# Kernel optimization log

Measured on AMD Instinct MI355X. Metric: run time of the kernel, lower is better.

## Reference

```python
import jax, jax.numpy as jnp
import numpy as np

B = 4096
D = 1024
NUM_CLASSES = 100
TEMPERATURE = 0.5
EPS = 1e-12  # matches F.normalize default eps


def setup_inputs() -> dict:
    key = jax.random.key(0)
    k1, k2, k3 = jax.random.split(key, 3)
    emb_i = jax.random.normal(k1, (B, D), dtype=jnp.float32)
    emb_j = jax.random.normal(k2, (B, D), dtype=jnp.float32)
    labels = jax.random.randint(k3, (B,), 0, NUM_CLASSES, dtype=jnp.int32)
    return {"emb_i": emb_i, "emb_j": emb_j, "labels": labels}


def _l2_normalize(x):
    # F.normalize(x, dim=1): x / max(||x||, eps)
    n = jnp.sqrt(jnp.sum(x * x, axis=1, keepdims=True))
    return x / jnp.maximum(n, EPS)


def reference(emb_i, emb_j, labels):
    z_i = _l2_normalize(emb_i)
    z_j = _l2_normalize(emb_j)
    reps = jnp.concatenate([z_i, z_j], axis=0)          # [2B, D]
    # cosine similarity of already-unit vectors == dot product (GEMM instead
    # of the O(N^2 D) broadcasted elementwise form in the torch code)
    sim = jnp.einsum("nd,md->nm", reps, reps)           # [2B, 2B]

    n2 = 2 * B
    neg_mask = 1.0 - jnp.eye(n2, dtype=sim.dtype)       # exclude self-pairs
    label_t = jnp.concatenate([labels, labels], axis=0)  # [2B]
    ws = (label_t[:, None] == label_t[None, :]).astype(sim.dtype) * neg_mask

    e = jnp.exp(sim / TEMPERATURE)                      # [2B, 2B]
    nominator = jnp.sum(ws * e, axis=1)                 # [2B]
    denominator = jnp.sum(neg_mask * e, axis=1)         # [2B]
    loss_partial = -jnp.log(nominator / denominator)
    return jnp.sum(loss_partial) / (2 * B)
```

## Files before the change

kernel.cpp:

```cpp
#include <hip/hip_runtime.h>
#include <hip/hip_bf16.h>
#include <hip/hip_fp8.h>


#define BHALF 4096
#define N2 8192
#define DK 1024
#define DKB 512
#define TILE 128
#define BKB 64
#define NTILE 64
#define NBLK 2080

typedef __attribute__((ext_vector_type(16))) float f32x16;
typedef __attribute__((ext_vector_type(4))) int v4i;
typedef __attribute__((ext_vector_type(8))) int v8i;
typedef unsigned char u8;
typedef unsigned short u16;

#define EXP_SCALE4 0.0028177637517362566f
#define UNIT_SCALE 0x7f7f7f7f

#define WAITVM(n) asm volatile("s_waitcnt vmcnt(" #n ")" ::: "memory")
#define BAR()     asm volatile("s_barrier" ::: "memory")

static __device__ __forceinline__ unsigned nib4(float x) {
    unsigned s = (__builtin_bit_cast(unsigned, x) >> 31) << 3;
    float a = fminf(fabsf(x), 6.0f);
    unsigned c;
    if (a < 2.0f)      c = (unsigned)lrintf(a * 2.0f);
    else if (a < 4.0f) c = (unsigned)lrintf(a) + 2u;
    else               c = (a < 5.0f) ? 6u : 7u;
    return s | c;
}

__global__ __launch_bounds__(256) void normalize_kernel(
    const float* __restrict__ emb_i, const float* __restrict__ emb_j,
    u16* __restrict__ reps, float* __restrict__ out) {
    int idx = blockIdx.x * 256 + threadIdx.x;
    if (idx == 0) out[0] = 0.0f;
    int r = blockIdx.x * 4 + (threadIdx.x >> 6);
    int lane = threadIdx.x & 63;
    const float* src = (r < BHALF) ? (emb_i + (size_t)r * DK)
                                   : (emb_j + (size_t)(r - BHALF) * DK);
    const float4* srcv = (const float4*)src;
    float4 v[4];
    float s = 0.f;
#pragma unroll
    for (int k = 0; k < 4; ++k) {
        v[k] = srcv[k * 64 + lane];
        s += v[k].x * v[k].x + v[k].y * v[k].y +
             v[k].z * v[k].z + v[k].w * v[k].w;
    }
#pragma unroll
    for (int m = 1; m <= 32; m <<= 1) s += __shfl_xor(s, m, 64);
    float scale = 32.0f / fmaxf(sqrtf(s), 1e-12f);
    u16* dst = reps + (size_t)r * 256;
#pragma unroll
    for (int k = 0; k < 4; ++k) {
        unsigned p = nib4(v[k].x * scale) |
                     (nib4(v[k].y * scale) << 4) |
                     (nib4(v[k].z * scale) << 8) |
                     (nib4(v[k].w * scale) << 12);
        dst[k * 64 + lane] = (u16)p;
    }
}

__global__ __launch_bounds__(256, 4) void gemm_loss_kernel(
    const u8* __restrict__ reps, const int* __restrict__ labels,
    float* __restrict__ parts) {
    __shared__ __align__(16) u8 A_s[2][TILE * BKB];
    __shared__ __align__(16) u8 B_s[2][TILE * BKB];
    __shared__ float red[2][2][128];

    int g = blockIdx.x;
    int rem = (g & 7) * 260 + (g >> 3);
    int bi = 0;
    while (rem >= NTILE - bi) { rem -= NTILE - bi; ++bi; }
    int bj = bi + rem;
    int rowBase = bi * TILE;
    int colBase = bj * TILE;

    int tid = threadIdx.x;
    int w = tid >> 6;
    int lane = tid & 63;
    int wm = w >> 1, wn = w & 1;
    int hk = lane >> 5;
    int l31 = lane & 31;

    f32x16 acc[2][2];
#pragma unroll
    for (int i = 0; i < 2; ++i)
#pragma unroll
        for (int j = 0; j < 2; ++j)
#pragma unroll
            for (int r = 0; r < 16; ++r) acc[i][j][r] = 0.0f;

    int srow = lane >> 2;
    int sbg = (lane & 3) ^ ((srow ^ (srow >> 2)) & 3);
    const u8* gA = reps + (size_t)(rowBase + w * 32 + srow) * DKB + sbg * 16;
    const u8* gB = reps + (size_t)(colBase + w * 32 + srow) * DKB + sbg * 16;

    int rswz = (l31 ^ (l31 >> 2)) & 3;
    unsigned aOff[2][2], bOff[2][2];
#pragma unroll
    for (int i = 0; i < 2; ++i) {
#pragma unroll
        for (int ks = 0; ks < 2; ++ks) {
            int ra = (wm * 64 + i * 32 + l31) * BKB;
            aOff[i][ks] = ra + (((ks * 2 + hk) ^ rswz) << 4);
            int rb = (wn * 64 + i * 32 + l31) * BKB;
            bOff[i][ks] = rb + (((ks * 2 + hk) ^ rswz) << 4);
        }
    }

#define STAGE(buf, kt)                                                       \
    {                                                                        \
        _Pragma("unroll")                                                    \
        for (int c = 0; c < 2; ++c) {                                        \
            int chunk = 2 * w + c;                                           \
            __builtin_amdgcn_global_load_lds(                                \
                (const __attribute__((address_space(1))) void*)              \
                    (gA + (size_t)c * 16 * DKB + (kt) * BKB),                \
                (__attribute__((address_space(3))) void*)                    \
                    &A_s[buf][chunk * 1024], 16, 0, 0);                      \
            __builtin_amdgcn_global_load_lds(                                \
                (const __attribute__((address_space(1))) void*)              \
                    (gB + (size_t)c * 16 * DKB + (kt) * BKB),                \
                (__attribute__((address_space(3))) void*)                    \
                    &B_s[buf][chunk * 1024], 16, 0, 0);                      \
        }                                                                    \
    }
#define COMPUTE(buf)                                                         \
    {                                                                        \
        _Pragma("unroll")                                                    \
        for (int ks = 0; ks < 2; ++ks) {                                     \
            v8i aF[2], bF[2];                                                \
            _Pragma("unroll")                                                \
            for (int i = 0; i < 2; ++i) {                                    \
                v4i a4 = *(const v4i*)&A_s[buf][aOff[i][ks]];                \
                aF[i] = __builtin_shufflevector(a4, a4, 0,1,2,3,0,1,2,3);    \
                v4i b4 = *(const v4i*)&B_s[buf][bOff[i][ks]];                \
                bF[i] = __builtin_shufflevector(b4, b4, 0,1,2,3,0,1,2,3);    \
            }                                                                \
            _Pragma("unroll")                                                \
            for (int i = 0; i < 2; ++i)                                      \
                _Pragma("unroll")                                            \
                for (int j = 0; j < 2; ++j)                                  \
                    acc[i][j] =                                              \
                        __builtin_amdgcn_mfma_scale_f32_32x32x64_f8f6f4(     \
                            aF[i], bF[j], acc[i][j], 4, 4,                   \
                            0, UNIT_SCALE, 0, UNIT_SCALE);                   \
        }                                                                    \
    }

    STAGE(0, 0)
    STAGE(1, 1)
    for (int kt = 0; kt < 4; kt += 2) {
        WAITVM(4); BAR();
        COMPUTE(0)
        BAR();
        STAGE(0, kt + 2)
        WAITVM(4); BAR();
        COMPUTE(1)
        BAR();
        STAGE(1, kt + 3)
    }
    WAITVM(4); BAR();
    COMPUTE(0)
    BAR();
    STAGE(0, 6)
    WAITVM(4); BAR();
    COMPUTE(1)
    BAR();
    STAGE(1, 7)
    WAITVM(4); BAR();
    COMPUTE(0)
    WAITVM(0); BAR();
    COMPUTE(1)
#undef STAGE
#undef COMPUTE

    bool offd = (bi != bj);
    int lc[2], gcol[2];
#pragma unroll
    for (int j = 0; j < 2; ++j) {
        gcol[j] = colBase + wn * 64 + j * 32 + l31;
        lc[j] = labels[gcol[j] & (BHALF - 1)];
    }
    float vD[32], vN[32];
    float colD[2] = {0.f, 0.f}, colN[2] = {0.f, 0.f};
#pragma unroll
    for (int i = 0; i < 2; ++i) {
#pragma unroll
        for (int reg = 0; reg < 16; ++reg) {
            int rowIn = (reg & 3) + 8 * (reg >> 2) + 4 * hk;
            int grow = rowBase + wm * 64 + i * 32 + rowIn;
            int labr = labels[grow & (BHALF - 1)];
            float rD = 0.f, rN = 0.f;
#pragma unroll
            for (int j = 0; j < 2; ++j) {
                float e = exp2f(acc[i][j][reg] * EXP_SCALE4);
                if (grow == gcol[j]) e = 0.f;
                bool m = (lc[j] == labr);
                rD += e; if (m) rN += e;
                colD[j] += e; if (m) colN[j] += e;
            }
            vD[i * 16 + reg] = rD;
            vN[i * 16 + reg] = rN;
        }
    }
#pragma unroll
    for (int step = 0; step < 5; ++step) {
        const int m = 16 >> step;
        const int h = 16 >> step;
        bool up = (l31 & m) != 0;
#pragma unroll
        for (int k = 0; k < h; ++k) {
            float sD = up ? vD[k] : vD[k + h];
            float sN = up ? vN[k] : vN[k + h];
            float kD = up ? vD[k + h] : vD[k];
            float kN = up ? vN[k + h] : vN[k];
            vD[k] = kD + __shfl_xor(sD, m, 64);
            vN[k] = kN + __shfl_xor(sN, m, 64);
        }
    }
    ((float*)red)[tid] = 0.0f;
    ((float*)red)[tid + 256] = 0.0f;
    __syncthreads();
    {
        int rowOff = wm * 64 + (l31 >> 4) * 32 +
                     ((l31 & 3) + 8 * ((l31 >> 2) & 3) + 4 * hk);
        atomicAdd(&red[0][0][rowOff], vN[0]);
        atomicAdd(&red[1][0][rowOff], vD[0]);
    }
    if (offd) {
#pragma unroll
        for (int j = 0; j < 2; ++j) {
            float cd = colD[j] + __shfl_xor(colD[j], 32, 64);
            float cn = colN[j] + __shfl_xor(colN[j], 32, 64);
            if (hk == 0) {
                int colOff = wn * 64 + j * 32 + l31;
                atomicAdd(&red[0][1][colOff], cn);
                atomicAdd(&red[1][1][colOff], cd);
            }
        }
    }
    __syncthreads();
    if (tid < 128) {
        parts[((size_t)bj * 2 + 0) * N2 + rowBase + tid] = red[0][0][tid];
        parts[((size_t)bj * 2 + 1) * N2 + rowBase + tid] = red[1][0][tid];
    } else if (offd) {
        int t2 = tid - 128;
        parts[((size_t)bi * 2 + 0) * N2 + colBase + t2] = red[0][1][t2];
        parts[((size_t)bi * 2 + 1) * N2 + colBase + t2] = red[1][1][t2];
    }
}

__global__ __launch_bounds__(256) void finalize_kernel(
    const float* __restrict__ parts, float* __restrict__ out) {
    int row = blockIdx.x * 256 + threadIdx.x;
    int t = threadIdx.x;
    float n = 0.f, d = 0.f;
#pragma unroll 8
    for (int s = 0; s < NTILE; ++s) {
        n += parts[((size_t)s * 2 + 0) * N2 + row];
        d += parts[((size_t)s * 2 + 1) * N2 + row];
    }
    float sv = logf(d) - logf(n);
#pragma unroll
    for (int m = 1; m <= 32; m <<= 1) sv += __shfl_xor(sv, m, 64);
    __shared__ float red[4];
    if ((t & 63) == 0) red[t >> 6] = sv;
    __syncthreads();
    if (t == 0)
        atomicAdd(out, (red[0] + red[1] + red[2] + red[3]) / (float)N2);
}

extern "C" void kernel_launch(void* const* d_in, const int* in_sizes, int n_in,
                              void* d_out, int out_size, void* d_ws, size_t ws_size,
                              hipStream_t stream) {
    const float* emb_i = (const float*)d_in[0];
    const float* emb_j = (const float*)d_in[1];
    const int* labels  = (const int*)d_in[2];
    float* out = (float*)d_out;

    char* ws = (char*)d_ws;
    u8* reps    = (u8*)ws;
    float* parts = (float*)(ws + (size_t)N2 * DKB);

    normalize_kernel<<<2048, 256, 0, stream>>>(emb_i, emb_j, (u16*)reps, out);
    gemm_loss_kernel<<<NBLK, 256, 0, stream>>>(reps, labels, parts);
    finalize_kernel<<<(N2 + 255) / 256, 256, 0, stream>>>(parts, out);
}
```

Before: 133.0 us.

## Restructure epilogue reduction, pack partials as float2, raw exp, MFMA priority

The epilogue's row reduction now runs per 32-row sub-tile, with the row-sum and numerator values packed into one 32-entry array that goes through a single butterfly. This lowers the number of live registers, and the lane halves end up holding N or D. Partial sums are stored as interleaved float2, so the finalize kernel issues one vector load per slice instead of two strided scalar loads. The change also adds an inline-asm v_exp_f32, wraps the MFMA issue in s_setprio, and leaves the upper halves of the fp4 operand vectors undefined to avoid register duplication. The risks are the correctness of the new lane-to-row mapping and the loss of denormal handling in the raw exp.

```diff
diff --git a/kernel.cpp b/kernel.cpp
--- a/kernel.cpp
+++ b/kernel.cpp
@@ -23,6 +23,12 @@
 
 #define WAITVM(n) asm volatile("s_waitcnt vmcnt(" #n ")" ::: "memory")
 #define BAR()     asm volatile("s_barrier" ::: "memory")
+
+static __device__ __forceinline__ float fexp2(float x) {
+    float r;
+    asm("v_exp_f32 %0, %1\n\ts_nop 1" : "=v"(r) : "v"(x));
+    return r;
+}
 
 static __device__ __forceinline__ unsigned nib4(float x) {
     unsigned s = (__builtin_bit_cast(unsigned, x) >> 31) << 3;
@@ -68,10 +74,10 @@
 
 __global__ __launch_bounds__(256, 4) void gemm_loss_kernel(
     const u8* __restrict__ reps, const int* __restrict__ labels,
-    float* __restrict__ parts) {
+    float2* __restrict__ parts) {
     __shared__ __align__(16) u8 A_s[2][TILE * BKB];
     __shared__ __align__(16) u8 B_s[2][TILE * BKB];
-    __shared__ float red[2][2][128];
+    __shared__ float2 red2[2][128];
 
     int g = blockIdx.x;
     int rem = (g & 7) * 260 + (g >> 3);
@@ -139,10 +145,11 @@
             _Pragma("unroll")                                                \
             for (int i = 0; i < 2; ++i) {                                    \
                 v4i a4 = *(const v4i*)&A_s[buf][aOff[i][ks]];                \
-                aF[i] = __builtin_shufflevector(a4, a4, 0,1,2,3,0,1,2,3);    \
+                aF[i] = __builtin_shufflevector(a4, a4, 0,1,2,3,-1,-1,-1,-1);\
                 v4i b4 = *(const v4i*)&B_s[buf][bOff[i][ks]];                \
-                bF[i] = __builtin_shufflevector(b4, b4, 0,1,2,3,0,1,2,3);    \
+                bF[i] = __builtin_shufflevector(b4, b4, 0,1,2,3,-1,-1,-1,-1);\
             }                                                                \
+            __builtin_amdgcn_s_setprio(1);                                   \
             _Pragma("unroll")                                                \
             for (int i = 0; i < 2; ++i)                                      \
                 _Pragma("unroll")                                            \
@@ -151,6 +158,7 @@
                         __builtin_amdgcn_mfma_scale_f32_32x32x64_f8f6f4(     \
                             aF[i], bF[j], acc[i][j], 4, 4,                   \
                             0, UNIT_SCALE, 0, UNIT_SCALE);                   \
+            __builtin_amdgcn_s_setprio(0);                                   \
         }                                                                    \
     }
 
@@ -188,10 +196,14 @@
         gcol[j] = colBase + wn * 64 + j * 32 + l31;
         lc[j] = labels[gcol[j] & (BHALF - 1)];
     }
-    float vD[32], vN[32];
+    ((float*)red2)[tid] = 0.0f;
+    ((float*)red2)[tid + 256] = 0.0f;
+    __syncthreads();
+
     float colD[2] = {0.f, 0.f}, colN[2] = {0.f, 0.f};
 #pragma unroll
     for (int i = 0; i < 2; ++i) {
+        float v[32];
 #pragma unroll
         for (int reg = 0; reg < 16; ++reg) {
             int rowIn = (reg & 3) + 8 * (reg >> 2) + 4 * hk;
@@ -200,39 +212,35 @@
             float rD = 0.f, rN = 0.f;
 #pragma unroll
             for (int j = 0; j < 2; ++j) {
-                float e = exp2f(acc[i][j][reg] * EXP_SCALE4);
+                float e = fexp2(acc[i][j][reg] * EXP_SCALE4);
                 if (grow == gcol[j]) e = 0.f;
                 bool m = (lc[j] == labr);
                 rD += e; if (m) rN += e;
                 colD[j] += e; if (m) colN[j] += e;
             }
-            vD[i * 16 + reg] = rD;
-            vN[i * 16 + reg] = rN;
-        }
-    }
-#pragma unroll
-    for (int step = 0; step < 5; ++step) {
-        const int m = 16 >> step;
-        const int h = 16 >> step;
-        bool up = (l31 & m) != 0;
-#pragma unroll
-        for (int k = 0; k < h; ++k) {
-            float sD = up ? vD[k] : vD[k + h];
-            float sN = up ? vN[k] : vN[k + h];
-            float kD = up ? vD[k + h] : vD[k];
-            float kN = up ? vN[k + h] : vN[k];
-            vD[k] = kD + __shfl_xor(sD, m, 64);
-            vN[k] = kN + __shfl_xor(sN, m, 64);
-        }
-    }
-    ((float*)red)[tid] = 0.0f;
-    ((float*)red)[tid + 256] = 0.0f;
-    __syncthreads();
-    {
-        int rowOff = wm * 64 + (l31 >> 4) * 32 +
-                     ((l31 & 3) + 8 * ((l31 >> 2) & 3) + 4 * hk);
-        atomicAdd(&red[0][0][rowOff], vN[0]);
-        atomicAdd(&red[1][0][rowOff], vD[0]);
+            v[reg] = rD;
+            v[16 + reg] = rN;
+        }
+#pragma unroll
+        for (int step = 0; step < 5; ++step) {
+            const int m = 16 >> step;
+            const int h = 16 >> step;
+            bool up = (l31 & m) != 0;
+#pragma unroll
+            for (int k = 0; k < h; ++k) {
+                float sV = up ? v[k] : v[k + h];
+                float kV = up ? v[k + h] : v[k];
+                v[k] = kV + __shfl_xor(sV, m, 64);
+            }
+        }
+        {
+            int reg = l31 & 15;
+            int rowOff = wm * 64 + i * 32 +
+                         ((reg & 3) + 8 * (reg >> 2) + 4 * hk);
+            float* cell = (l31 & 16) ? &red2[0][rowOff].x
+                                     : &red2[0][rowOff].y;
+            atomicAdd(cell, v[0]);
+        }
     }
     if (offd) {
 #pragma unroll
@@ -241,31 +249,29 @@
             float cn = colN[j] + __shfl_xor(colN[j], 32, 64);
             if (hk == 0) {
                 int colOff = wn * 64 + j * 32 + l31;
-                atomicAdd(&red[0][1][colOff], cn);
-                atomicAdd(&red[1][1][colOff], cd);
+                atomicAdd(&red2[1][colOff].x, cn);
+                atomicAdd(&red2[1][colOff].y, cd);
             }
         }
     }
     __syncthreads();
     if (tid < 128) {
-        parts[((size_t)bj * 2 + 0) * N2 + rowBase + tid] = red[0][0][tid];
-        parts[((size_t)bj * 2 + 1) * N2 + rowBase + tid] = red[1][0][tid];
+        parts[(size_t)bj * N2 + rowBase + tid] = red2[0][tid];
     } else if (offd) {
-        int t2 = tid - 128;
-        parts[((size_t)bi * 2 + 0) * N2 + colBase + t2] = red[0][1][t2];
-        parts[((size_t)bi * 2 + 1) * N2 + colBase + t2] = red[1][1][t2];
+        parts[(size_t)bi * N2 + colBase + tid - 128] = red2[1][tid - 128];
     }
 }
 
 __global__ __launch_bounds__(256) void finalize_kernel(
-    const float* __restrict__ parts, float* __restrict__ out) {
+    const float2* __restrict__ parts, float* __restrict__ out) {
     int row = blockIdx.x * 256 + threadIdx.x;
     int t = threadIdx.x;
     float n = 0.f, d = 0.f;
 #pragma unroll 8
     for (int s = 0; s < NTILE; ++s) {
-        n += parts[((size_t)s * 2 + 0) * N2 + row];
-        d += parts[((size_t)s * 2 + 1) * N2 + row];
+        float2 p = parts[(size_t)s * N2 + row];
+        n += p.x;
+        d += p.y;
     }
     float sv = logf(d) - logf(n);
 #pragma unroll
@@ -286,8 +292,8 @@
     float* out = (float*)d_out;
 
     char* ws = (char*)d_ws;
-    u8* reps    = (u8*)ws;
-    float* parts = (float*)(ws + (size_t)N2 * DKB);
+    u8* reps     = (u8*)ws;
+    float2* parts = (float2*)(ws + (size_t)N2 * DKB);
 
     normalize_kernel<<<2048, 256, 0, stream>>>(emb_i, emb_j, (u16*)reps, out);
     gemm_loss_kernel<<<NBLK, 256, 0, stream>>>(reps, labels, parts);
```

New measurement: 124.2 us. -6.6%, faster.
